# Kernel tuning notes

Measured on AMD Instinct MI355X. Metric: run time of the kernel, lower is better.

Reference implementation:

```python
import jax, jax.numpy as jnp
import numpy as np

B, S, HID, NH = 2, 2048, 1024, 16
HD = HID // NH
BASE = 10000.0


def _rope_tables(seq_len, head_dim):
    i = jnp.arange(0, head_dim, 2, dtype=jnp.float32)
    theta = BASE ** (-i / head_dim)
    pos = jnp.arange(seq_len, dtype=jnp.float32)
    m_theta = jnp.outer(pos, theta)  # [S, HD/2]
    cos = jnp.repeat(jnp.cos(m_theta), 2, axis=1)  # [S, HD]
    sin = jnp.repeat(jnp.sin(m_theta), 2, axis=1)
    return cos, sin


def _apply_rope(x, cos, sin):
    # x: [B, NH, S, HD]; interleaved rotation: (-x1, x0, -x3, x2, ...)
    x_even = x[..., 0::2]
    x_odd = x[..., 1::2]
    inv_x = jnp.stack((-x_odd, x_even), axis=-1).reshape(x.shape)
    return x * cos[None, None] + inv_x * sin[None, None]


def setup_inputs() -> dict:
    key = jax.random.key(0)
    ks = jax.random.split(key, 7)
    q = jax.random.normal(ks[0], (B, S, HID), dtype=jnp.float32)
    k = jax.random.normal(ks[1], (B, S, HID), dtype=jnp.float32)
    v = jax.random.normal(ks[2], (B, S, HID), dtype=jnp.float32)
    scale = 1.0 / np.sqrt(HID)
    Wq = jax.random.normal(ks[3], (HID, HID), dtype=jnp.float32) * scale
    Wk = jax.random.normal(ks[4], (HID, HID), dtype=jnp.float32) * scale
    Wv = jax.random.normal(ks[5], (HID, HID), dtype=jnp.float32) * scale
    Wo = jax.random.normal(ks[6], (HID, HID), dtype=jnp.float32) * scale
    mask = jnp.triu(jnp.ones((S, S), dtype=bool), k=1)[None, None]  # causal, True = masked
    return {"q": q, "k": k, "v": v, "mask": mask,
            "Wq": Wq, "Wk": Wk, "Wv": Wv, "Wo": Wo}


def reference(q, k, v, mask, Wq, Wk, Wv, Wo):
    cos, sin = _rope_tables(S, HD)
    # Linear (torch stores weight as [out, in]; y = x @ W.T)
    qh = (q @ Wq.T).reshape(B, S, NH, HD).transpose(0, 2, 1, 3)
    kh = (k @ Wk.T).reshape(B, S, NH, HD).transpose(0, 2, 1, 3)
    vh = (v @ Wv.T).reshape(B, S, NH, HD).transpose(0, 2, 1, 3)
    qh = _apply_rope(qh, cos, sin)
    kh = _apply_rope(kh, cos, sin)
    scores = jnp.einsum("bhqd,bhkd->bhqk", qh, kh) / np.sqrt(HD)
    neg_min = jnp.finfo(jnp.float32).min
    scores = jnp.where(mask, neg_min, scores)
    attn = jax.nn.softmax(scores, axis=-1)
    out = jnp.einsum("bhqk,bhkd->bhqd", attn, vh)  # [B,NH,S,HD]
    out = out.transpose(0, 2, 1, 3).reshape(B, S, HID)
    return out @ Wo.T
```

## Files before the change

### kernel.cpp

```cpp
#include <hip/hip_runtime.h>

#define S_LEN 2048
#define HIDN  1024
#define NHEAD 16
#define HDIM  64
#define MROWS 4096
#define KDIM  1024
#define NDIM  1024

typedef __attribute__((ext_vector_type(8))) short bf16x8;
typedef __attribute__((ext_vector_type(4))) float f32x4;

static __device__ __forceinline__ ushort f2bf(float f) {
    unsigned int u = __float_as_uint(f);
    u = (u + 0x7fffu + ((u >> 16) & 1u)) >> 16;
    return (ushort)u;
}
static __device__ __forceinline__ float bf2f(ushort u) {
    return __uint_as_float(((unsigned int)u) << 16);
}

static __device__ __forceinline__ void gload16(const ushort* g, ushort* l) {
    __builtin_amdgcn_global_load_lds(
        (const __attribute__((address_space(1))) unsigned int*)g,
        (__attribute__((address_space(3))) unsigned int*)l, 16, 0, 0);
}

__global__ __launch_bounds__(256) void prep_kernel(
    const float* __restrict__ q, const float* __restrict__ k,
    const float* __restrict__ v, const float* __restrict__ Wq,
    const float* __restrict__ Wk, const float* __restrict__ Wv,
    const float* __restrict__ Wo,
    ushort* __restrict__ qb, ushort* __restrict__ kb, ushort* __restrict__ vb,
    ushort* __restrict__ Wqb, ushort* __restrict__ Wkb, ushort* __restrict__ Wvb,
    ushort* __restrict__ Wob,
    float* __restrict__ rc, float* __restrict__ rs)
{
    const long Q4 = (long)MROWS * KDIM / 4;
    const long W4 = (long)NDIM * KDIM / 4;
    if (blockIdx.x < 16384) {
        long i = (long)blockIdx.x * 256 + threadIdx.x;
        const float* src; ushort* dst; long off;
        if (i < Q4)          { src = q; dst = qb; off = i; }
        else if (i < 2 * Q4) { src = k; dst = kb; off = i - Q4; }
        else if (i < 3 * Q4) { src = v; dst = vb; off = i - 2 * Q4; }
        else {
            long t = i - 3 * Q4;
            int wsel = (int)(t >> 18);
            off = t & (W4 - 1);
            src = (wsel == 0) ? Wq : (wsel == 1) ? Wk : (wsel == 2) ? Wv : Wo;
            dst = (wsel == 0) ? Wqb : (wsel == 1) ? Wkb : (wsel == 2) ? Wvb : Wob;
        }
        float4 vv = ((const float4*)src)[off];
        ushort4 o;
        o.x = f2bf(vv.x); o.y = f2bf(vv.y); o.z = f2bf(vv.z); o.w = f2bf(vv.w);
        ((ushort4*)dst)[off] = o;
    } else {
        int idx = (blockIdx.x - 16384) * 256 + threadIdx.x;
        int s  = idx >> 5;
        int jp = idx & 31;
        float theta = expf(-(float)(2 * jp) * (9.210340371976184f / 64.0f));
        float ang = (float)s * theta;
        float sv, cv;
        sincosf(ang, &sv, &cv);
        rc[idx] = cv;
        rs[idx] = sv;
    }
}

static __device__ __forceinline__ void gemm_mainloop(
    const ushort* __restrict__ A, const ushort* __restrict__ W,
    ushort* As, ushort* Bs, f32x4 (&acc)[2][4],
    int m0, int n0, int tid)
{
    const int lane = tid & 63, wid = tid >> 6;
    const int wm = wid & 1, wn = wid >> 1;
    const int quad = lane >> 4, l15 = lane & 15;

    for (int k0 = 0; k0 < KDIM; k0 += 64) {
        __syncthreads();
#pragma unroll
        for (int rr = 0; rr < 2; ++rr) {
            int sidx = tid + rr * 256;
            int row = sidx >> 3;
            int g = (sidx & 7) ^ (row & 7);
            gload16(A + (size_t)(m0 + row) * KDIM + k0 + g * 8, As + sidx * 8);
        }
#pragma unroll
        for (int rr = 0; rr < 4; ++rr) {
            int sidx = tid + rr * 256;
            int row = sidx >> 3;
            int g = (sidx & 7) ^ (row & 7);
            gload16(W + (size_t)(n0 + row) * KDIM + k0 + g * 8, Bs + sidx * 8);
        }
        __syncthreads();

#pragma unroll
        for (int ks = 0; ks < 2; ++ks) {
            bf16x8 af[2], bfr[4];
#pragma unroll
            for (int i = 0; i < 2; ++i) {
                int row = wm * 32 + i * 16 + l15;
                int gg = ((ks << 2) | quad) ^ (row & 7);
                af[i] = *(const bf16x8*)&As[row * 64 + gg * 8];
            }
#pragma unroll
            for (int j = 0; j < 4; ++j) {
                int row = wn * 64 + j * 16 + l15;
                int gg = ((ks << 2) | quad) ^ (row & 7);
                bfr[j] = *(const bf16x8*)&Bs[row * 64 + gg * 8];
            }
#pragma unroll
            for (int i = 0; i < 2; ++i)
#pragma unroll
                for (int j = 0; j < 4; ++j)
                    acc[i][j] = __builtin_amdgcn_mfma_f32_16x16x32_bf16(
                        af[i], bfr[j], acc[i][j], 0, 0, 0);
        }
    }
}

__global__ __launch_bounds__(256) void gemm_qkv(
    const ushort* __restrict__ qb, const ushort* __restrict__ kb,
    const ushort* __restrict__ vb,
    const ushort* __restrict__ Wqb, const ushort* __restrict__ Wkb,
    const ushort* __restrict__ Wvb,
    ushort* __restrict__ Qh, ushort* __restrict__ Kh, ushort* __restrict__ Vt,
    const float* __restrict__ rc, const float* __restrict__ rs)
{
    __shared__ __align__(16) ushort As[64 * 64];
    __shared__ __align__(16) ushort Bs[128 * 64];

    const int tid = threadIdx.x;
    const int lane = tid & 63, wid = tid >> 6;
    const int wm = wid & 1, wn = wid >> 1;
    const int quad = lane >> 4, l15 = lane & 15;
    const int z = blockIdx.z;

    const ushort* A; const ushort* W; int m0, n0;
    if (z == 2) {
        m0 = ((int)blockIdx.y * 2 + ((int)blockIdx.x >> 5)) * 64;
        n0 = ((int)blockIdx.x & 31) * 128;
        A = Wvb; W = vb;
    } else {
        m0 = blockIdx.x * 64; n0 = blockIdx.y * 128;
        A = (z == 0) ? qb : kb;
        W = (z == 0) ? Wqb : Wkb;
    }

    f32x4 acc[2][4];
#pragma unroll
    for (int i = 0; i < 2; ++i)
#pragma unroll
        for (int j = 0; j < 4; ++j) acc[i][j] = 0.0f;

    gemm_mainloop(A, W, As, Bs, acc, m0, n0, tid);

    if (z != 2) {
        ushort* out = (z == 0) ? Qh : Kh;
        const float scale = (z == 0) ? 0.18033688011112042f : 1.0f;
#pragma unroll
        for (int i = 0; i < 2; ++i)
#pragma unroll
            for (int j = 0; j < 4; ++j)
#pragma unroll
                for (int r = 0; r < 4; ++r) {
                    int m = m0 + wm * 32 + i * 16 + quad * 4 + r;
                    int n = n0 + wn * 64 + j * 16 + l15;
                    float v = acc[i][j][r];
                    int b = m >> 11, s = m & (S_LEN - 1);
                    int h = n >> 6, d = n & 63;
                    int pidx = s * 32 + (d >> 1);
                    float cv = rc[pidx], sv = rs[pidx];
                    float partner = __shfl_xor(v, 1);
                    v = (d & 1) ? (v * cv + partner * sv)
                                : (v * cv - partner * sv);
                    out[((size_t)((b * NHEAD + h) * S_LEN + s)) * HDIM + d] =
                        f2bf(v * scale);
                }
    } else {
#pragma unroll
        for (int i = 0; i < 2; ++i)
#pragma unroll
            for (int j = 0; j < 4; ++j)
#pragma unroll
                for (int r = 0; r < 4; ++r) {
                    int m = m0 + wm * 32 + i * 16 + quad * 4 + r;
                    int n = n0 + wn * 64 + j * 16 + l15;
                    int h = m >> 6, d = m & 63;
                    int b = n >> 11, s = n & (S_LEN - 1);
                    Vt[((size_t)((b * NHEAD + h) * HDIM + d)) * S_LEN + s] =
                        f2bf(acc[i][j][r]);
                }
    }
}

__global__ __launch_bounds__(256) void gemm_out(
    const ushort* __restrict__ A, const ushort* __restrict__ W,
    float* __restrict__ out)
{
    __shared__ __align__(16) ushort As[64 * 64];
    __shared__ __align__(16) ushort Bs[128 * 64];

    const int tid = threadIdx.x;
    const int lane = tid & 63, wid = tid >> 6;
    const int wm = wid & 1, wn = wid >> 1;
    const int quad = lane >> 4, l15 = lane & 15;
    const int m0 = blockIdx.x * 64, n0 = blockIdx.y * 128;

    f32x4 acc[2][4];
#pragma unroll
    for (int i = 0; i < 2; ++i)
#pragma unroll
        for (int j = 0; j < 4; ++j) acc[i][j] = 0.0f;

    gemm_mainloop(A, W, As, Bs, acc, m0, n0, tid);

#pragma unroll
    for (int i = 0; i < 2; ++i)
#pragma unroll
        for (int j = 0; j < 4; ++j)
#pragma unroll
            for (int r = 0; r < 4; ++r) {
                int m = m0 + wm * 32 + i * 16 + quad * 4 + r;
                int n = n0 + wn * 64 + j * 16 + l15;
                out[(size_t)m * NDIM + n] = acc[i][j][r];
            }
}

__global__ __launch_bounds__(256) void attn_mfma(
    const ushort* __restrict__ Qh, const ushort* __restrict__ Kh,
    const ushort* __restrict__ Vt,
    ushort* __restrict__ O0, ushort* __restrict__ O1,
    float* __restrict__ L0, float* __restrict__ L1)
{
    __shared__ __align__(16) ushort Ks[64 * 64];
    __shared__ __align__(16) ushort Vs[64 * 64];
    __shared__ __align__(16) ushort Ps[64 * 72];

    const int tid = threadIdx.x;
    const int lane = tid & 63, w = tid >> 6;
    const int quad = lane >> 4, l15 = lane & 15;
    const int id = blockIdx.x;
    const int h = id & 15, y = (id >> 4) & 31, b = id >> 9;
    const size_t hoff = (size_t)(b * NHEAD + h) * S_LEN * HDIM;

    bf16x8 ones;
#pragma unroll
    for (int i = 0; i < 8; ++i) ones[i] = (short)0x3F80;

#pragma unroll
    for (int seg = 0; seg < 2; ++seg) {
        const int qt = seg ? (31 - y) : y;
        const int lo = seg ? ((33 - y) >> 1) : 0;
        const int hi = seg ? (32 - y) : ((y + 2) >> 1);
        const int q0 = qt * 64;

        bf16x8 qf[2];
#pragma unroll
        for (int ks = 0; ks < 2; ++ks)
            qf[ks] = *(const bf16x8*)(Qh + hoff +
                (size_t)(q0 + w * 16 + l15) * HDIM + ks * 32 + quad * 8);

        f32x4 Oa[4];
        f32x4 Lacc = 0.0f;
#pragma unroll
        for (int j = 0; j < 4; ++j) Oa[j] = 0.0f;

        const int rowq = q0 + w * 16 + quad * 4;

        for (int kt = lo; kt < hi; ++kt) {
            const int k0 = kt * 64;
            const bool diag = (kt == qt);
            __syncthreads();
#pragma unroll
            for (int rr = 0; rr < 2; ++rr) {
                int sidx = tid + rr * 256;
                int row = sidx >> 3;
                int g = (sidx & 7) ^ (row & 7);
                gload16(Kh + hoff + (size_t)(k0 + row) * HDIM + g * 8, Ks + sidx * 8);
                gload16(Vt + hoff + (size_t)row * S_LEN + k0 + g * 8, Vs + sidx * 8);
            }
            __syncthreads();

            f32x4 Sa[4];
#pragma unroll
            for (int j = 0; j < 4; ++j) Sa[j] = 0.0f;
#pragma unroll
            for (int ks = 0; ks < 2; ++ks) {
                const int p = ((ks << 2) | quad) ^ (l15 & 7);
                bf16x8 kf[4];
#pragma unroll
                for (int j = 0; j < 4; ++j)
                    kf[j] = *(const bf16x8*)&Ks[(j * 16 + l15) * 64 + p * 8];
#pragma unroll
                for (int j = 0; j < 4; ++j)
                    Sa[j] = __builtin_amdgcn_mfma_f32_16x16x32_bf16(qf[ks], kf[j],
                                                                    Sa[j], 0, 0, 0);
            }

#pragma unroll
            for (int j = 0; j < 4; ++j) {
#pragma unroll
                for (int r = 0; r < 4; ++r) {
                    float p = exp2f(Sa[j][r]);
                    if (diag) {
                        int key = k0 + j * 16 + l15;
                        if (key > rowq + r) p = 0.f;
                    }
                    Ps[(w * 16 + quad * 4 + r) * 72 + j * 16 + l15] =
                        (ushort)(__float_as_uint(p) >> 16);
                }
            }

#pragma unroll
            for (int ks = 0; ks < 2; ++ks) {
                const int p = ((ks << 2) | quad) ^ (l15 & 7);
                bf16x8 pf = *(const bf16x8*)&Ps[(w * 16 + l15) * 72 + ks * 32 + quad * 8];
                bf16x8 vf[4];
#pragma unroll
                for (int j = 0; j < 4; ++j)
                    vf[j] = *(const bf16x8*)&Vs[(j * 16 + l15) * 64 + p * 8];
#pragma unroll
                for (int j = 0; j < 4; ++j)
                    Oa[j] = __builtin_amdgcn_mfma_f32_16x16x32_bf16(pf, vf[j],
                                                                    Oa[j], 0, 0, 0);
                Lacc = __builtin_amdgcn_mfma_f32_16x16x32_bf16(pf, ones, Lacc, 0, 0, 0);
            }
        }

        ushort* Op = seg ? O1 : O0;
        float*  Lp = seg ? L1 : L0;
        const size_t rbase = ((size_t)(b * NHEAD + h) * S_LEN + rowq);
#pragma unroll
        for (int r = 0; r < 4; ++r) {
#pragma unroll
            for (int j = 0; j < 4; ++j)
                Op[(rbase + r) * HDIM + j * 16 + l15] = f2bf(Oa[j][r]);
            if (l15 == 0) Lp[rbase + r] = Lacc[r];
        }
    }
}

__global__ __launch_bounds__(256) void combine_kernel(
    const ushort* __restrict__ O0, const ushort* __restrict__ O1,
    const float* __restrict__ L0, const float* __restrict__ L1,
    ushort* __restrict__ AO)
{
    int flat = blockIdx.x * 256 + threadIdx.x;
    int row = flat >> 4;
    int dq = (flat & 15) * 4;
    int bh = row >> 11, s = row & (S_LEN - 1);
    int b = bh >> 4, h = bh & 15;
    ushort4 a = *(const ushort4*)(O0 + (size_t)row * HDIM + dq);
    ushort4 c = *(const ushort4*)(O1 + (size_t)row * HDIM + dq);
    float inv = 1.0f / (L0[row] + L1[row]);
    ushort4 o;
    o.x = f2bf((bf2f(a.x) + bf2f(c.x)) * inv);
    o.y = f2bf((bf2f(a.y) + bf2f(c.y)) * inv);
    o.z = f2bf((bf2f(a.z) + bf2f(c.z)) * inv);
    o.w = f2bf((bf2f(a.w) + bf2f(c.w)) * inv);
    *(ushort4*)(AO + ((size_t)(b * S_LEN + s)) * HIDN + h * HDIM + dq) = o;
}

extern "C" void kernel_launch(void* const* d_in, const int* in_sizes, int n_in,
                              void* d_out, int out_size, void* d_ws, size_t ws_size,
                              hipStream_t stream) {
    const float* qf  = (const float*)d_in[0];
    const float* kf  = (const float*)d_in[1];
    const float* vf  = (const float*)d_in[2];
    const float* Wqf = (const float*)d_in[4];
    const float* Wkf = (const float*)d_in[5];
    const float* Wvf = (const float*)d_in[6];
    const float* Wof = (const float*)d_in[7];
    float* out = (float*)d_out;

    char* wsp = (char*)d_ws;
    float* rc = (float*)wsp;            wsp += 65536 * 4;
    float* rs = (float*)wsp;            wsp += 65536 * 4;
    ushort* qb  = (ushort*)wsp;         wsp += (size_t)MROWS * KDIM * 2;
    ushort* kb  = (ushort*)wsp;         wsp += (size_t)MROWS * KDIM * 2;
    ushort* vb  = (ushort*)wsp;         wsp += (size_t)MROWS * KDIM * 2;
    ushort* Wqb = (ushort*)wsp;         wsp += (size_t)NDIM * KDIM * 2;
    ushort* Wkb = (ushort*)wsp;         wsp += (size_t)NDIM * KDIM * 2;
    ushort* Wvb = (ushort*)wsp;         wsp += (size_t)NDIM * KDIM * 2;
    ushort* Wob = (ushort*)wsp;         wsp += (size_t)NDIM * KDIM * 2;
    ushort* Qh  = (ushort*)wsp;         wsp += (size_t)MROWS * HIDN * 2;
    ushort* Kh  = (ushort*)wsp;         wsp += (size_t)MROWS * HIDN * 2;
    ushort* Vt  = (ushort*)wsp;         wsp += (size_t)MROWS * HIDN * 2;
    ushort* AO  = (ushort*)wsp;

    ushort* O0 = qb;
    ushort* O1 = kb;
    float*  L0 = (float*)vb;
    float*  L1 = (float*)vb + 65536;

    prep_kernel<<<16640, 256, 0, stream>>>(qf, kf, vf, Wqf, Wkf, Wvf, Wof,
                                           qb, kb, vb, Wqb, Wkb, Wvb, Wob, rc, rs);

    gemm_qkv<<<dim3(64, 8, 3), 256, 0, stream>>>(
        qb, kb, vb, Wqb, Wkb, Wvb, Qh, Kh, Vt, rc, rs);

    attn_mfma<<<1024, 256, 0, stream>>>(Qh, Kh, Vt, O0, O1, L0, L1);

    combine_kernel<<<4096, 256, 0, stream>>>(O0, O1, L0, L1, AO);

    gemm_out<<<dim3(64, 8), 256, 0, stream>>>(AO, Wob, out);
}
```

Before: 222.7 us.

## Split each causal query tile's key range into three blocks instead of pairing tiles

```diff
diff --git a/kernel.cpp b/kernel.cpp
--- a/kernel.cpp
+++ b/kernel.cpp
@@ -231,8 +231,8 @@
 __global__ __launch_bounds__(256) void attn_mfma(
     const ushort* __restrict__ Qh, const ushort* __restrict__ Kh,
     const ushort* __restrict__ Vt,
-    ushort* __restrict__ O0, ushort* __restrict__ O1,
-    float* __restrict__ L0, float* __restrict__ L1)
+    ushort* __restrict__ O0, ushort* __restrict__ O1, ushort* __restrict__ O2,
+    float* __restrict__ L0, float* __restrict__ L1, float* __restrict__ L2)
 {
     __shared__ __align__(16) ushort Ks[64 * 64];
     __shared__ __align__(16) ushort Vs[64 * 64];
@@ -242,109 +242,122 @@
     const int lane = tid & 63, w = tid >> 6;
     const int quad = lane >> 4, l15 = lane & 15;
     const int id = blockIdx.x;
-    const int h = id & 15, y = (id >> 4) & 31, b = id >> 9;
+    const int h = id & 15, b = (id >> 4) & 1, t = id >> 5;
+
+    const int g3 = t / 3;
+    const int qt = 31 - g3;
+    const int j3 = t - g3 * 3;
+    const int n = qt + 1;
+    const int lo = (n * j3) / 3;
+    const int hi = (n * (j3 + 1)) / 3;
+    const int q0 = qt * 64;
     const size_t hoff = (size_t)(b * NHEAD + h) * S_LEN * HDIM;
 
     bf16x8 ones;
 #pragma unroll
     for (int i = 0; i < 8; ++i) ones[i] = (short)0x3F80;
 
-#pragma unroll
-    for (int seg = 0; seg < 2; ++seg) {
-        const int qt = seg ? (31 - y) : y;
-        const int lo = seg ? ((33 - y) >> 1) : 0;
-        const int hi = seg ? (32 - y) : ((y + 2) >> 1);
-        const int q0 = qt * 64;
-
-        bf16x8 qf[2];
-#pragma unroll
-        for (int ks = 0; ks < 2; ++ks)
-            qf[ks] = *(const bf16x8*)(Qh + hoff +
-                (size_t)(q0 + w * 16 + l15) * HDIM + ks * 32 + quad * 8);
-
-        f32x4 Oa[4];
-        f32x4 Lacc = 0.0f;
-#pragma unroll
-        for (int j = 0; j < 4; ++j) Oa[j] = 0.0f;
-
-        const int rowq = q0 + w * 16 + quad * 4;
-
-        for (int kt = lo; kt < hi; ++kt) {
-            const int k0 = kt * 64;
-            const bool diag = (kt == qt);
-            __syncthreads();
-#pragma unroll
-            for (int rr = 0; rr < 2; ++rr) {
-                int sidx = tid + rr * 256;
-                int row = sidx >> 3;
-                int g = (sidx & 7) ^ (row & 7);
-                gload16(Kh + hoff + (size_t)(k0 + row) * HDIM + g * 8, Ks + sidx * 8);
-                gload16(Vt + hoff + (size_t)row * S_LEN + k0 + g * 8, Vs + sidx * 8);
+    bf16x8 qf[2];
+#pragma unroll
+    for (int ks = 0; ks < 2; ++ks)
+        qf[ks] = *(const bf16x8*)(Qh + hoff +
+            (size_t)(q0 + w * 16 + l15) * HDIM + ks * 32 + quad * 8);
+
+    f32x4 Oa[4];
+    f32x4 Lacc = 0.0f;
+#pragma unroll
+    for (int j = 0; j < 4; ++j) Oa[j] = 0.0f;
+
+    const int rowq = q0 + w * 16 + quad * 4;
+
+    const ushort* kg[2]; const ushort* vg[2];
+#pragma unroll
+    for (int rr = 0; rr < 2; ++rr) {
+        int sidx = tid + rr * 256;
+        int row = sidx >> 3;
+        int gsw = (sidx & 7) ^ (row & 7);
+        kg[rr] = Kh + hoff + (size_t)(lo * 64 + row) * HDIM + gsw * 8;
+        vg[rr] = Vt + hoff + (size_t)row * S_LEN + lo * 64 + gsw * 8;
+    }
+    ushort* psw = Ps + (w * 16 + quad * 4) * 72;
+    const ushort* psr = Ps + (w * 16 + l15) * 72;
+
+    for (int kt = lo; kt < hi; ++kt) {
+        const int k0 = kt * 64;
+        const bool diag = (kt == qt);
+        __syncthreads();
+#pragma unroll
+        for (int rr = 0; rr < 2; ++rr) {
+            int sidx = tid + rr * 256;
+            gload16(kg[rr], Ks + sidx * 8);
+            gload16(vg[rr], Vs + sidx * 8);
+            kg[rr] += 64 * HDIM;
+            vg[rr] += 64;
+        }
+        __syncthreads();
+
+        f32x4 Sa[4];
+#pragma unroll
+        for (int j = 0; j < 4; ++j) Sa[j] = 0.0f;
+#pragma unroll
+        for (int ks = 0; ks < 2; ++ks) {
+            const int p = ((ks << 2) | quad) ^ (l15 & 7);
+            bf16x8 kf[4];
+#pragma unroll
+            for (int j = 0; j < 4; ++j)
+                kf[j] = *(const bf16x8*)&Ks[(j * 16 + l15) * 64 + p * 8];
+#pragma unroll
+            for (int j = 0; j < 4; ++j)
+                Sa[j] = __builtin_amdgcn_mfma_f32_16x16x32_bf16(qf[ks], kf[j],
+                                                                Sa[j], 0, 0, 0);
+        }
+
+#pragma unroll
+        for (int j = 0; j < 4; ++j) {
+#pragma unroll
+            for (int r = 0; r < 4; ++r) {
+                float p = exp2f(Sa[j][r]);
+                if (diag) {
+                    int key = k0 + j * 16 + l15;
+                    if (key > rowq + r) p = 0.f;
+                }
+                psw[r * 72 + j * 16 + l15] = (ushort)(__float_as_uint(p) >> 16);
             }
-            __syncthreads();
-
-            f32x4 Sa[4];
-#pragma unroll
-            for (int j = 0; j < 4; ++j) Sa[j] = 0.0f;
-#pragma unroll
-            for (int ks = 0; ks < 2; ++ks) {
-                const int p = ((ks << 2) | quad) ^ (l15 & 7);
-                bf16x8 kf[4];
-#pragma unroll
-                for (int j = 0; j < 4; ++j)
-                    kf[j] = *(const bf16x8*)&Ks[(j * 16 + l15) * 64 + p * 8];
-#pragma unroll
-                for (int j = 0; j < 4; ++j)
-                    Sa[j] = __builtin_amdgcn_mfma_f32_16x16x32_bf16(qf[ks], kf[j],
-                                                                    Sa[j], 0, 0, 0);
-            }
-
-#pragma unroll
-            for (int j = 0; j < 4; ++j) {
-#pragma unroll
-                for (int r = 0; r < 4; ++r) {
-                    float p = exp2f(Sa[j][r]);
-                    if (diag) {
-                        int key = k0 + j * 16 + l15;
-                        if (key > rowq + r) p = 0.f;
-                    }
-                    Ps[(w * 16 + quad * 4 + r) * 72 + j * 16 + l15] =
-                        (ushort)(__float_as_uint(p) >> 16);
-                }
-            }
-
-#pragma unroll
-            for (int ks = 0; ks < 2; ++ks) {
-                const int p = ((ks << 2) | quad) ^ (l15 & 7);
-                bf16x8 pf = *(const bf16x8*)&Ps[(w * 16 + l15) * 72 + ks * 32 + quad * 8];
-                bf16x8 vf[4];
-#pragma unroll
-                for (int j = 0; j < 4; ++j)
-                    vf[j] = *(const bf16x8*)&Vs[(j * 16 + l15) * 64 + p * 8];
-#pragma unroll
-                for (int j = 0; j < 4; ++j)
-                    Oa[j] = __builtin_amdgcn_mfma_f32_16x16x32_bf16(pf, vf[j],
-                                                                    Oa[j], 0, 0, 0);
-                Lacc = __builtin_amdgcn_mfma_f32_16x16x32_bf16(pf, ones, Lacc, 0, 0, 0);
-            }
-        }
-
-        ushort* Op = seg ? O1 : O0;
-        float*  Lp = seg ? L1 : L0;
-        const size_t rbase = ((size_t)(b * NHEAD + h) * S_LEN + rowq);
-#pragma unroll
-        for (int r = 0; r < 4; ++r) {
-#pragma unroll
-            for (int j = 0; j < 4; ++j)
-                Op[(rbase + r) * HDIM + j * 16 + l15] = f2bf(Oa[j][r]);
-            if (l15 == 0) Lp[rbase + r] = Lacc[r];
-        }
+        }
+
+#pragma unroll
+        for (int ks = 0; ks < 2; ++ks) {
+            const int p = ((ks << 2) | quad) ^ (l15 & 7);
+            bf16x8 pf = *(const bf16x8*)&psr[ks * 32 + quad * 8];
+            bf16x8 vf[4];
+#pragma unroll
+            for (int j = 0; j < 4; ++j)
+                vf[j] = *(const bf16x8*)&Vs[(j * 16 + l15) * 64 + p * 8];
+#pragma unroll
+            for (int j = 0; j < 4; ++j)
+                Oa[j] = __builtin_amdgcn_mfma_f32_16x16x32_bf16(pf, vf[j],
+                                                                Oa[j], 0, 0, 0);
+            Lacc = __builtin_amdgcn_mfma_f32_16x16x32_bf16(pf, ones, Lacc, 0, 0, 0);
+        }
+    }
+
+    ushort* Op = (j3 == 0) ? O0 : (j3 == 1) ? O1 : O2;
+    float*  Lp = (j3 == 0) ? L0 : (j3 == 1) ? L1 : L2;
+    const size_t rbase = ((size_t)(b * NHEAD + h) * S_LEN + rowq);
+#pragma unroll
+    for (int r = 0; r < 4; ++r) {
+#pragma unroll
+        for (int j = 0; j < 4; ++j)
+            Op[(rbase + r) * HDIM + j * 16 + l15] = f2bf(Oa[j][r]);
+        if (l15 == 0) Lp[rbase + r] = Lacc[r];
     }
 }
 
 __global__ __launch_bounds__(256) void combine_kernel(
     const ushort* __restrict__ O0, const ushort* __restrict__ O1,
+    const ushort* __restrict__ O2,
     const float* __restrict__ L0, const float* __restrict__ L1,
+    const float* __restrict__ L2,
     ushort* __restrict__ AO)
 {
     int flat = blockIdx.x * 256 + threadIdx.x;
@@ -354,12 +367,13 @@
     int b = bh >> 4, h = bh & 15;
     ushort4 a = *(const ushort4*)(O0 + (size_t)row * HDIM + dq);
     ushort4 c = *(const ushort4*)(O1 + (size_t)row * HDIM + dq);
-    float inv = 1.0f / (L0[row] + L1[row]);
+    ushort4 e = *(const ushort4*)(O2 + (size_t)row * HDIM + dq);
+    float inv = 1.0f / (L0[row] + L1[row] + L2[row]);
     ushort4 o;
-    o.x = f2bf((bf2f(a.x) + bf2f(c.x)) * inv);
-    o.y = f2bf((bf2f(a.y) + bf2f(c.y)) * inv);
-    o.z = f2bf((bf2f(a.z) + bf2f(c.z)) * inv);
-    o.w = f2bf((bf2f(a.w) + bf2f(c.w)) * inv);
+    o.x = f2bf((bf2f(a.x) + bf2f(c.x) + bf2f(e.x)) * inv);
+    o.y = f2bf((bf2f(a.y) + bf2f(c.y) + bf2f(e.y)) * inv);
+    o.z = f2bf((bf2f(a.z) + bf2f(c.z) + bf2f(e.z)) * inv);
+    o.w = f2bf((bf2f(a.w) + bf2f(c.w) + bf2f(e.w)) * inv);
     *(ushort4*)(AO + ((size_t)(b * S_LEN + s)) * HIDN + h * HDIM + dq) = o;
 }
 
@@ -392,8 +406,10 @@
 
     ushort* O0 = qb;
     ushort* O1 = kb;
-    float*  L0 = (float*)vb;
-    float*  L1 = (float*)vb + 65536;
+    ushort* O2 = vb;
+    float*  L0 = rc;
+    float*  L1 = rs;
+    float*  L2 = (float*)Wqb;
 
     prep_kernel<<<16640, 256, 0, stream>>>(qf, kf, vf, Wqf, Wkf, Wvf, Wof,
                                            qb, kb, vb, Wqb, Wkb, Wvb, Wob, rc, rs);
@@ -401,9 +417,9 @@
     gemm_qkv<<<dim3(64, 8, 3), 256, 0, stream>>>(
         qb, kb, vb, Wqb, Wkb, Wvb, Qh, Kh, Vt, rc, rs);
 
-    attn_mfma<<<1024, 256, 0, stream>>>(Qh, Kh, Vt, O0, O1, L0, L1);
-
-    combine_kernel<<<4096, 256, 0, stream>>>(O0, O1, L0, L1, AO);
+    attn_mfma<<<3072, 256, 0, stream>>>(Qh, Kh, Vt, O0, O1, O2, L0, L1, L2);
+
+    combine_kernel<<<4096, 256, 0, stream>>>(O0, O1, O2, L0, L1, L2, AO);
 
     gemm_out<<<dim3(64, 8), 256, 0, stream>>>(AO, Wob, out);
 }
```

Result: faster. 216.3 us (-2.9%).
